# Kernel tuning notes

Measured on AMD Instinct MI355X. Metric: run time of the kernel, lower is better.

Reference implementation:

```python
import jax, jax.numpy as jnp
import numpy as np
from math import sqrt as msqrt

D_MODEL, D_FF, N_HEADS, D_K, D_V = 1024, 4096, 16, 64, 64
NEG = -1e9

def gelu_erf(x):
    return 0.5 * x * (1.0 + jax.lax.erf(x / msqrt(2.0)))

def layer_norm(x, g, b, eps=1e-5):
    mu = jnp.mean(x, axis=-1, keepdims=True)
    var = jnp.mean(jnp.square(x - mu), axis=-1, keepdims=True)
    return (x - mu) * jax.lax.rsqrt(var + eps) * g + b

def setup_inputs() -> dict:
    key = jax.random.key(0)
    ks = jax.random.split(key, 12)
    B, S = 2, 2048
    s = lambda fan_in: 1.0 / msqrt(fan_in)
    inp = {
        "x": jax.random.normal(ks[0], (B, S, D_MODEL), dtype=jnp.float32),
        "pad_mask": jnp.zeros((B, S, S), dtype=bool),
        "W_Q": jax.random.uniform(ks[1], (D_MODEL, N_HEADS * D_K), minval=-s(D_MODEL), maxval=s(D_MODEL)),
        "W_K": jax.random.uniform(ks[2], (D_MODEL, N_HEADS * D_K), minval=-s(D_MODEL), maxval=s(D_MODEL)),
        "W_V": jax.random.uniform(ks[3], (D_MODEL, N_HEADS * D_V), minval=-s(D_MODEL), maxval=s(D_MODEL)),
        "W_O": jax.random.uniform(ks[4], (N_HEADS * D_V, D_MODEL), minval=-s(N_HEADS * D_V), maxval=s(N_HEADS * D_V)),
        "fc1_w": jax.random.uniform(ks[5], (D_MODEL, D_FF), minval=-s(D_MODEL), maxval=s(D_MODEL)),
        "fc1_b": jax.random.uniform(ks[6], (D_FF,), minval=-s(D_MODEL), maxval=s(D_MODEL)),
        "fc2_w": jax.random.uniform(ks[7], (D_FF, D_MODEL), minval=-s(D_FF), maxval=s(D_FF)),
        "fc2_b": jax.random.uniform(ks[8], (D_MODEL,), minval=-s(D_FF), maxval=s(D_FF)),
        "ln1_g": jnp.ones((D_MODEL,), jnp.float32),
        "ln1_b": jnp.zeros((D_MODEL,), jnp.float32),
        "ln2_g": jnp.ones((D_MODEL,), jnp.float32),
        "ln2_b": jnp.zeros((D_MODEL,), jnp.float32),
    }
    return inp

def reference(x, pad_mask, W_Q, W_K, W_V, W_O, fc1_w, fc1_b, fc2_w, fc2_b,
              ln1_g, ln1_b, ln2_g, ln2_b):
    B, S, _ = x.shape
    # --- pre-norm MHA ---
    residual = x
    h = layer_norm(x, ln1_g, ln1_b)
    q = (h @ W_Q).reshape(B, S, N_HEADS, D_K).transpose(0, 2, 1, 3)  # [B,H,S,dk]
    k = (h @ W_K).reshape(B, S, N_HEADS, D_K).transpose(0, 2, 1, 3)
    v = (h @ W_V).reshape(B, S, N_HEADS, D_V).transpose(0, 2, 1, 3)
    scores = jnp.einsum("bhqd,bhkd->bhqk", q, k) / msqrt(D_K)
    scores = jnp.where(pad_mask[:, None, :, :], NEG, scores)
    attn = jax.nn.softmax(scores, axis=-1)
    ctx = jnp.einsum("bhqk,bhkd->bhqd", attn, v)
    ctx = ctx.transpose(0, 2, 1, 3).reshape(B, S, N_HEADS * D_V)
    x = ctx @ W_O + residual
    # --- pre-norm FFN (dropout is identity at inference) ---
    residual = x
    h = layer_norm(x, ln2_g, ln2_b)
    h = gelu_erf(h @ fc1_w + fc1_b)
    x = h @ fc2_w + fc2_b + residual
    return x
```

## Files before the change

kernel.cpp:

```cpp
#include <hip/hip_runtime.h>
#include <hip/hip_bf16.h>
#include <math.h>

#define DI __device__ __forceinline__

typedef short s16x8 __attribute__((ext_vector_type(8)));
typedef unsigned short u16x8_t __attribute__((ext_vector_type(8)));
typedef float f32x4 __attribute__((ext_vector_type(4)));

static constexpr int T_TOK = 4096;
static constexpr int DM    = 1024;
static constexpr int DFF   = 4096;
static constexpr int S_LEN = 2048;
static constexpr int NB    = 2;
static constexpr int LDQ   = 3072;

DI unsigned short f2bf(float f) {
    unsigned int u = __builtin_bit_cast(unsigned int, f);
    u += 0x7fffu + ((u >> 16) & 1u);
    return (unsigned short)(u >> 16);
}

DI float gelu_f(float x) {
    return 0.5f * x * (1.0f + erff(x * 0.70710678118654752440f));
}

DI int swz(int r) { return (r & 7) ^ ((r >> 3) & 7); }

DI void gload_lds16(const void* g, void* l) {
    __builtin_amdgcn_global_load_lds((const unsigned int*)g, (unsigned int*)l, 16, 0, 0);
}

__global__ __launch_bounds__(256) void tcvt_kernel(const float* __restrict__ in,
                                                   unsigned short* __restrict__ out,
                                                   int K, int N) {
    __shared__ float tile[32][33];
    const int tx = threadIdx.x & 31, ty = threadIdx.x >> 5;
    const int k0 = blockIdx.y * 32, n0 = blockIdx.x * 32;
#pragma unroll
    for (int i = 0; i < 4; ++i) {
        int k = ty + i * 8;
        tile[k][tx] = in[(size_t)(k0 + k) * N + n0 + tx];
    }
    __syncthreads();
#pragma unroll
    for (int i = 0; i < 4; ++i) {
        int n = ty + i * 8;
        out[(size_t)(n0 + n) * K + k0 + tx] = f2bf(tile[tx][n]);
    }
}

__global__ __launch_bounds__(256) void ln_kernel(const float* __restrict__ x,
                                                 const float* __restrict__ g,
                                                 const float* __restrict__ b,
                                                 unsigned short* __restrict__ out) {
    int row = blockIdx.x;
    int t = threadIdx.x;
    const float4 v = reinterpret_cast<const float4*>(x + (size_t)row * DM)[t];
    float s = v.x + v.y + v.z + v.w;
    float s2 = v.x * v.x + v.y * v.y + v.z * v.z + v.w * v.w;
#pragma unroll
    for (int m = 1; m < 64; m <<= 1) { s += __shfl_xor(s, m, 64); s2 += __shfl_xor(s2, m, 64); }
    __shared__ float red[8];
    int w = t >> 6;
    if ((t & 63) == 0) { red[w] = s; red[4 + w] = s2; }
    __syncthreads();
    s = red[0] + red[1] + red[2] + red[3];
    s2 = red[4] + red[5] + red[6] + red[7];
    float mu = s * (1.0f / DM);
    float var = s2 * (1.0f / DM) - mu * mu;
    float rs = rsqrtf(var + 1e-5f);
    float4 gv = reinterpret_cast<const float4*>(g)[t];
    float4 bv = reinterpret_cast<const float4*>(b)[t];
    ushort4 ov = make_ushort4(f2bf((v.x - mu) * rs * gv.x + bv.x),
                              f2bf((v.y - mu) * rs * gv.y + bv.y),
                              f2bf((v.z - mu) * rs * gv.z + bv.z),
                              f2bf((v.w - mu) * rs * gv.w + bv.w));
    reinterpret_cast<ushort4*>(out + (size_t)row * DM)[t] = ov;
}

template <int EPI>
__global__ __launch_bounds__(256) void gemm_kernel(const unsigned short* __restrict__ A,
                                                   const unsigned short* __restrict__ Bt,
                                                   const float* __restrict__ bias,
                                                   const float* __restrict__ resid,
                                                   void* __restrict__ Cv, int M, int N, int K) {
    __shared__ unsigned short Asm[128][32];
    __shared__ unsigned short Bsm[128][32];
    const int t = threadIdx.x, lane = t & 63, w = t >> 6;
    const int wr = w >> 1, wc = w & 1;
    const int m0 = blockIdx.y * 128, n0 = blockIdx.x * 128;
    const int c = lane & 15, g = lane >> 4;
    const int srow = lane >> 2, scol = (lane & 3) * 8;

    f32x4 acc[4][4] = {};
    const unsigned short* Ab = A + (size_t)m0 * K;
    const unsigned short* Bb = Bt + (size_t)n0 * K;

    for (int k0 = 0; k0 < K; k0 += 32) {
        __syncthreads();
#pragma unroll
        for (int cc = 0; cc < 2; ++cc) {
            int ch = 2 * w + cc;
            int r = ch * 16 + srow;
            gload_lds16(Ab + (size_t)r * K + k0 + scol, &Asm[ch * 16][0]);
            gload_lds16(Bb + (size_t)r * K + k0 + scol, &Bsm[ch * 16][0]);
        }
        __syncthreads();
        s16x8 af[4], bf[4];
#pragma unroll
        for (int i = 0; i < 4; ++i)
            af[i] = *reinterpret_cast<const s16x8*>(&Asm[wr * 64 + i * 16 + c][g * 8]);
#pragma unroll
        for (int n = 0; n < 4; ++n)
            bf[n] = *reinterpret_cast<const s16x8*>(&Bsm[wc * 64 + n * 16 + c][g * 8]);
#pragma unroll
        for (int i = 0; i < 4; ++i)
#pragma unroll
            for (int n = 0; n < 4; ++n)
                acc[i][n] = __builtin_amdgcn_mfma_f32_16x16x32_bf16(af[i], bf[n], acc[i][n], 0, 0, 0);
    }

    const int crow = g * 4;
#pragma unroll
    for (int i = 0; i < 4; ++i) {
#pragma unroll
        for (int n = 0; n < 4; ++n) {
            const int col = n0 + wc * 64 + n * 16 + c;
#pragma unroll
            for (int j = 0; j < 4; ++j) {
                const int row = m0 + wr * 64 + i * 16 + crow + j;
                float v = acc[i][n][j];
                if constexpr (EPI == 2) v = gelu_f(v + bias[col]);
                if constexpr (EPI == 3) v = v + bias[col] + resid[(size_t)row * N + col];
                if constexpr (EPI == 1) v = v + resid[(size_t)row * N + col];
                if constexpr (EPI == 4) v = (col < 1024) ? v * 0.125f : v;
                if constexpr (EPI == 2 || EPI == 4)
                    ((unsigned short*)Cv)[(size_t)row * N + col] = f2bf(v);
                else
                    ((float*)Cv)[(size_t)row * N + col] = v;
            }
        }
    }
}

__global__ __launch_bounds__(256) void attn_kernel(const unsigned short* __restrict__ QKV,
                                                   const unsigned char* __restrict__ mask,
                                                   unsigned short* __restrict__ O) {
    const int qt = blockIdx.x, h = blockIdx.y, b = blockIdx.z;
    const int t = threadIdx.x, lane = t & 63, w = t >> 6;
    const int c = lane & 15, g = lane >> 4;
    const int crow = g * 4;
    const int qb0 = qt * 64;
    const int qw = qb0 + w * 16;

    __shared__ unsigned short Ksm[64][64];
    __shared__ unsigned short VsmT[64][64];
    __shared__ unsigned short Psm[4][16][64];
    __shared__ unsigned char Msm[64][64];
    __shared__ int mflag[4];

    s16x8 qf[2];
    {
        const unsigned short* qp = QKV + (size_t)(b * S_LEN + qw + c) * LDQ + h * 64 + g * 8;
        qf[0] = *reinterpret_cast<const s16x8*>(qp);
        qf[1] = *reinterpret_cast<const s16x8*>(qp + 32);
    }

    float mrow[4] = {-3e38f, -3e38f, -3e38f, -3e38f};
    float lrow[4] = {0.f, 0.f, 0.f, 0.f};
    f32x4 oacc[4] = {};

    const int vtok = t >> 2;
    const int vd0 = (t & 3) * 16;
    const unsigned char* mbase = mask + (size_t)b * S_LEN * S_LEN + (size_t)(qb0 + vtok) * S_LEN + vd0;
    const unsigned short* kg = QKV + 1024;
    const unsigned short* vg = QKV + 2048;

    for (int kt = 0; kt < S_LEN; kt += 64) {
        __syncthreads();
#pragma unroll
        for (int cc = 0; cc < 2; ++cc) {
            int ch = 2 * w + cc;
            int r = ch * 8 + (lane >> 3);
            int slot = (lane & 7) ^ swz(r);
            gload_lds16(kg + (size_t)(b * S_LEN + kt + r) * LDQ + h * 64 + slot * 8,
                        &Ksm[ch * 8][0]);
        }
        u16x8_t v0, v1;
        {
            const unsigned short* vp = vg + (size_t)(b * S_LEN + kt + vtok) * LDQ + h * 64 + vd0;
            v0 = *reinterpret_cast<const u16x8_t*>(vp);
            v1 = *reinterpret_cast<const u16x8_t*>(vp + 8);
        }
        uint4 mv = *reinterpret_cast<const uint4*>(mbase + kt);
        unsigned mor = mv.x | mv.y | mv.z | mv.w;
        int anyw = __any(mor != 0);
        if (lane == 0) mflag[w] = anyw;
#pragma unroll
        for (int e = 0; e < 16; ++e) {
            int d = vd0 + e;
            unsigned short val = (e < 8) ? (unsigned short)v0[e] : (unsigned short)v1[e - 8];
            int byte = d * 128 + ((vtok * 2) ^ (swz(d) << 4));
            *(unsigned short*)((char*)&VsmT[0][0] + byte) = val;
        }
        __syncthreads();
        const int anym = mflag[0] | mflag[1] | mflag[2] | mflag[3];
        if (anym) {
            *reinterpret_cast<uint4*>(&Msm[vtok][vd0]) = mv;
            __syncthreads();
        }

        f32x4 s[4] = {};
#pragma unroll
        for (int kh = 0; kh < 2; ++kh) {
#pragma unroll
            for (int kb = 0; kb < 4; ++kb) {
                int key = kb * 16 + c;
                int byte = key * 128 + (((kh * 4 + g) ^ swz(key)) << 4);
                s16x8 kf = *(const s16x8*)((const char*)&Ksm[0][0] + byte);
                s[kb] = __builtin_amdgcn_mfma_f32_16x16x32_bf16(qf[kh], kf, s[kb], 0, 0, 0);
            }
        }
        if (anym) {
#pragma unroll
            for (int kb = 0; kb < 4; ++kb)
#pragma unroll
                for (int jr = 0; jr < 4; ++jr)
                    if (Msm[w * 16 + crow + jr][kb * 16 + c]) s[kb][jr] = -1e9f;
        }

        float corr[4];
#pragma unroll
        for (int jr = 0; jr < 4; ++jr) {
            float tm = fmaxf(fmaxf(s[0][jr], s[1][jr]), fmaxf(s[2][jr], s[3][jr]));
#pragma unroll
            for (int m = 1; m < 16; m <<= 1) tm = fmaxf(tm, __shfl_xor(tm, m, 16));
            float mnew = fmaxf(mrow[jr], tm);
            corr[jr] = __expf(mrow[jr] - mnew);
            mrow[jr] = mnew;
            float ps = 0.f;
#pragma unroll
            for (int kb = 0; kb < 4; ++kb) {
                float p = __expf(s[kb][jr] - mnew);
                s[kb][jr] = p;
                ps += p;
            }
#pragma unroll
            for (int m = 1; m < 16; m <<= 1) ps += __shfl_xor(ps, m, 16);
            lrow[jr] = lrow[jr] * corr[jr] + ps;
        }
#pragma unroll
        for (int nb = 0; nb < 4; ++nb)
#pragma unroll
            for (int jr = 0; jr < 4; ++jr) oacc[nb][jr] *= corr[jr];

#pragma unroll
        for (int kb = 0; kb < 4; ++kb)
#pragma unroll
            for (int jr = 0; jr < 4; ++jr) {
                int row = crow + jr;
                int byte = row * 128 + ((((kb * 16 + c) * 2)) ^ (swz(row) << 4));
                *(unsigned short*)((char*)&Psm[w][0][0] + byte) = f2bf(s[kb][jr]);
            }
#pragma unroll
        for (int kh = 0; kh < 2; ++kh) {
            int pbyte = c * 128 + (((kh * 4 + g) ^ swz(c)) << 4);
            s16x8 pf = *(const s16x8*)((const char*)&Psm[w][0][0] + pbyte);
#pragma unroll
            for (int nb = 0; nb < 4; ++nb) {
                int d = nb * 16 + c;
                int byte = d * 128 + (((kh * 4 + g) ^ swz(d)) << 4);
                s16x8 vf = *(const s16x8*)((const char*)&VsmT[0][0] + byte);
                oacc[nb] = __builtin_amdgcn_mfma_f32_16x16x32_bf16(pf, vf, oacc[nb], 0, 0, 0);
            }
        }
    }

    float inv[4];
#pragma unroll
    for (int jr = 0; jr < 4; ++jr) inv[jr] = lrow[jr] > 0.f ? 1.0f / lrow[jr] : 0.f;
#pragma unroll
    for (int nb = 0; nb < 4; ++nb) {
#pragma unroll
        for (int jr = 0; jr < 4; ++jr) {
            const size_t oo = (size_t)(b * S_LEN + qw + crow + jr) * DM + h * 64 + nb * 16 + c;
            O[oo] = f2bf(oacc[nb][jr] * inv[jr]);
        }
    }
}

extern "C" void kernel_launch(void* const* d_in, const int* in_sizes, int n_in,
                              void* d_out, int out_size, void* d_ws, size_t ws_size,
                              hipStream_t stream) {
    (void)in_sizes; (void)n_in; (void)out_size; (void)ws_size;
    const float* x   = (const float*)d_in[0];
    const unsigned char* mask = (const unsigned char*)d_in[1];
    const float* WQ  = (const float*)d_in[2];
    const float* WK  = (const float*)d_in[3];
    const float* WV  = (const float*)d_in[4];
    const float* WO  = (const float*)d_in[5];
    const float* F1W = (const float*)d_in[6];
    const float* F1B = (const float*)d_in[7];
    const float* F2W = (const float*)d_in[8];
    const float* F2B = (const float*)d_in[9];
    const float* L1G = (const float*)d_in[10];
    const float* L1B = (const float*)d_in[11];
    const float* L2G = (const float*)d_in[12];
    const float* L2B = (const float*)d_in[13];
    float* out = (float*)d_out;

    char* ws = (char*)d_ws;
    size_t off = 0;
    auto alloc = [&](size_t bytes) -> void* {
        void* p = ws + off;
        off += (bytes + 255) & ~(size_t)255;
        return p;
    };
    unsigned short* h1    = (unsigned short*)alloc((size_t)T_TOK * DM * 2);
    unsigned short* qkv   = (unsigned short*)alloc((size_t)T_TOK * LDQ * 2);
    unsigned short* ctx   = (unsigned short*)alloc((size_t)T_TOK * DM * 2);
    float*          x2    = (float*)alloc((size_t)T_TOK * DM * 4);
    unsigned short* h2    = (unsigned short*)alloc((size_t)T_TOK * DM * 2);
    unsigned short* h3    = (unsigned short*)alloc((size_t)T_TOK * DFF * 2);
    unsigned short* WQKVt = (unsigned short*)alloc((size_t)LDQ * DM * 2);
    unsigned short* WOt   = (unsigned short*)alloc((size_t)DM * DM * 2);
    unsigned short* F1Wt  = (unsigned short*)alloc((size_t)DFF * DM * 2);
    unsigned short* F2Wt  = (unsigned short*)alloc((size_t)DM * DFF * 2);

    dim3 t32(DM / 32, DM / 32);
    tcvt_kernel<<<t32, 256, 0, stream>>>(WQ, WQKVt, DM, DM);
    tcvt_kernel<<<t32, 256, 0, stream>>>(WK, WQKVt + (size_t)DM * DM, DM, DM);
    tcvt_kernel<<<t32, 256, 0, stream>>>(WV, WQKVt + (size_t)2 * DM * DM, DM, DM);
    tcvt_kernel<<<t32, 256, 0, stream>>>(WO, WOt, DM, DM);
    tcvt_kernel<<<dim3(DFF / 32, DM / 32), 256, 0, stream>>>(F1W, F1Wt, DM, DFF);
    tcvt_kernel<<<dim3(DM / 32, DFF / 32), 256, 0, stream>>>(F2W, F2Wt, DFF, DM);

    ln_kernel<<<T_TOK, 256, 0, stream>>>(x, L1G, L1B, h1);

    gemm_kernel<4><<<dim3(LDQ / 128, T_TOK / 128), 256, 0, stream>>>(h1, WQKVt, nullptr, nullptr,
                                                                     qkv, T_TOK, LDQ, DM);

    attn_kernel<<<dim3(S_LEN / 64, 16, NB), 256, 0, stream>>>(qkv, mask, ctx);

    gemm_kernel<1><<<dim3(DM / 128, T_TOK / 128), 256, 0, stream>>>(ctx, WOt, nullptr, x, x2,
                                                                    T_TOK, DM, DM);

    ln_kernel<<<T_TOK, 256, 0, stream>>>(x2, L2G, L2B, h2);

    gemm_kernel<2><<<dim3(DFF / 128, T_TOK / 128), 256, 0, stream>>>(h2, F1Wt, F1B, nullptr, h3,
                                                                     T_TOK, DFF, DM);
    gemm_kernel<3><<<dim3(DM / 128, T_TOK / 128), 256, 0, stream>>>(h3, F2Wt, F2B, x2, out,
                                                                    T_TOK, DM, DFF);
}
```

Before: 523.3 us.

## Write V transposed from QKV GEMM, double-buffer attention loads, narrow N-tiles for small GEMMs

The QKV GEMM epilogue now writes Q/K into a 2048-wide buffer and V transposed into a separate [dim][token] buffer. The attention kernel can then load V with async global-to-LDS copies instead of doing a per-element register transpose. Attention K/V tiles and mask loads are double-buffered so the next tile is fetched while the current one is computed. The N=1024 GEMMs (output projection and FC2) use 64-wide N tiles to launch twice as many blocks. Costs are strided scalar stores for the transposed V write and extra LDS for the double buffers.

New measurement: 522.9 us. About the same (-0.1%).

```diff
diff --git a/kernel.cpp b/kernel.cpp
--- a/kernel.cpp
+++ b/kernel.cpp
@@ -13,7 +13,7 @@
 static constexpr int DFF   = 4096;
 static constexpr int S_LEN = 2048;
 static constexpr int NB    = 2;
-static constexpr int LDQ   = 3072;
+static constexpr int LDK   = 2048;
 
 DI unsigned short f2bf(float f) {
     unsigned int u = __builtin_bit_cast(unsigned int, f);
@@ -79,21 +79,24 @@
     reinterpret_cast<ushort4*>(out + (size_t)row * DM)[t] = ov;
 }
 
-template <int EPI>
+template <int EPI, int BN>
 __global__ __launch_bounds__(256) void gemm_kernel(const unsigned short* __restrict__ A,
                                                    const unsigned short* __restrict__ Bt,
                                                    const float* __restrict__ bias,
                                                    const float* __restrict__ resid,
-                                                   void* __restrict__ Cv, int M, int N, int K) {
+                                                   void* __restrict__ Cv, void* __restrict__ Cv2,
+                                                   int M, int N, int K) {
+    constexpr int NN = BN / 32;
+    constexpr int BCH = BN / 64;
     __shared__ unsigned short Asm[128][32];
-    __shared__ unsigned short Bsm[128][32];
+    __shared__ unsigned short Bsm[BN][32];
     const int t = threadIdx.x, lane = t & 63, w = t >> 6;
     const int wr = w >> 1, wc = w & 1;
-    const int m0 = blockIdx.y * 128, n0 = blockIdx.x * 128;
+    const int m0 = blockIdx.y * 128, n0 = blockIdx.x * BN;
     const int c = lane & 15, g = lane >> 4;
     const int srow = lane >> 2, scol = (lane & 3) * 8;
 
-    f32x4 acc[4][4] = {};
+    f32x4 acc[4][NN] = {};
     const unsigned short* Ab = A + (size_t)m0 * K;
     const unsigned short* Bb = Bt + (size_t)n0 * K;
 
@@ -104,20 +107,25 @@
             int ch = 2 * w + cc;
             int r = ch * 16 + srow;
             gload_lds16(Ab + (size_t)r * K + k0 + scol, &Asm[ch * 16][0]);
+        }
+#pragma unroll
+        for (int cc = 0; cc < BCH; ++cc) {
+            int ch = BCH * w + cc;
+            int r = ch * 16 + srow;
             gload_lds16(Bb + (size_t)r * K + k0 + scol, &Bsm[ch * 16][0]);
         }
         __syncthreads();
-        s16x8 af[4], bf[4];
+        s16x8 af[4], bf[NN];
 #pragma unroll
         for (int i = 0; i < 4; ++i)
             af[i] = *reinterpret_cast<const s16x8*>(&Asm[wr * 64 + i * 16 + c][g * 8]);
 #pragma unroll
-        for (int n = 0; n < 4; ++n)
-            bf[n] = *reinterpret_cast<const s16x8*>(&Bsm[wc * 64 + n * 16 + c][g * 8]);
+        for (int n = 0; n < NN; ++n)
+            bf[n] = *reinterpret_cast<const s16x8*>(&Bsm[wc * (BN / 2) + n * 16 + c][g * 8]);
 #pragma unroll
         for (int i = 0; i < 4; ++i)
 #pragma unroll
-            for (int n = 0; n < 4; ++n)
+            for (int n = 0; n < NN; ++n)
                 acc[i][n] = __builtin_amdgcn_mfma_f32_16x16x32_bf16(af[i], bf[n], acc[i][n], 0, 0, 0);
     }
 
@@ -125,26 +133,36 @@
 #pragma unroll
     for (int i = 0; i < 4; ++i) {
 #pragma unroll
-        for (int n = 0; n < 4; ++n) {
-            const int col = n0 + wc * 64 + n * 16 + c;
+        for (int n = 0; n < NN; ++n) {
+            const int col = n0 + wc * (BN / 2) + n * 16 + c;
 #pragma unroll
             for (int j = 0; j < 4; ++j) {
                 const int row = m0 + wr * 64 + i * 16 + crow + j;
                 float v = acc[i][n][j];
-                if constexpr (EPI == 2) v = gelu_f(v + bias[col]);
-                if constexpr (EPI == 3) v = v + bias[col] + resid[(size_t)row * N + col];
-                if constexpr (EPI == 1) v = v + resid[(size_t)row * N + col];
-                if constexpr (EPI == 4) v = (col < 1024) ? v * 0.125f : v;
-                if constexpr (EPI == 2 || EPI == 4)
+                if constexpr (EPI == 2) {
+                    v = gelu_f(v + bias[col]);
                     ((unsigned short*)Cv)[(size_t)row * N + col] = f2bf(v);
-                else
+                } else if constexpr (EPI == 3) {
+                    v = v + bias[col] + resid[(size_t)row * N + col];
                     ((float*)Cv)[(size_t)row * N + col] = v;
-            }
-        }
-    }
-}
-
-__global__ __launch_bounds__(256) void attn_kernel(const unsigned short* __restrict__ QKV,
+                } else if constexpr (EPI == 1) {
+                    v = v + resid[(size_t)row * N + col];
+                    ((float*)Cv)[(size_t)row * N + col] = v;
+                } else {
+                    if (col < 2048) {
+                        float vv = (col < 1024) ? v * 0.125f : v;
+                        ((unsigned short*)Cv)[(size_t)row * LDK + col] = f2bf(vv);
+                    } else {
+                        ((unsigned short*)Cv2)[(size_t)(col - 2048) * T_TOK + row] = f2bf(v);
+                    }
+                }
+            }
+        }
+    }
+}
+
+__global__ __launch_bounds__(256) void attn_kernel(const unsigned short* __restrict__ QK,
+                                                   const unsigned short* __restrict__ Vt,
                                                    const unsigned char* __restrict__ mask,
                                                    unsigned short* __restrict__ O) {
     const int qt = blockIdx.x, h = blockIdx.y, b = blockIdx.z;
@@ -154,15 +172,14 @@
     const int qb0 = qt * 64;
     const int qw = qb0 + w * 16;
 
-    __shared__ unsigned short Ksm[64][64];
-    __shared__ unsigned short VsmT[64][64];
+    __shared__ unsigned short Ksm[2][64][64];
+    __shared__ unsigned short Vsm[2][64][64];
     __shared__ unsigned short Psm[4][16][64];
     __shared__ unsigned char Msm[64][64];
-    __shared__ int mflag[4];
 
     s16x8 qf[2];
     {
-        const unsigned short* qp = QKV + (size_t)(b * S_LEN + qw + c) * LDQ + h * 64 + g * 8;
+        const unsigned short* qp = QK + (size_t)(b * S_LEN + qw + c) * LDK + h * 64 + g * 8;
         qf[0] = *reinterpret_cast<const s16x8*>(qp);
         qf[1] = *reinterpret_cast<const s16x8*>(qp + 32);
     }
@@ -173,42 +190,39 @@
 
     const int vtok = t >> 2;
     const int vd0 = (t & 3) * 16;
-    const unsigned char* mbase = mask + (size_t)b * S_LEN * S_LEN + (size_t)(qb0 + vtok) * S_LEN + vd0;
-    const unsigned short* kg = QKV + 1024;
-    const unsigned short* vg = QKV + 2048;
-
-    for (int kt = 0; kt < S_LEN; kt += 64) {
-        __syncthreads();
+    const unsigned char* mcol = mask + (size_t)b * S_LEN * S_LEN + (size_t)(qb0 + vtok) * S_LEN + vd0;
+    const unsigned short* kg = QK + 1024;
+    const int srow8 = lane >> 3, sslot = lane & 7;
+
+    auto stage = [&](int buf, int kt) {
 #pragma unroll
         for (int cc = 0; cc < 2; ++cc) {
             int ch = 2 * w + cc;
-            int r = ch * 8 + (lane >> 3);
-            int slot = (lane & 7) ^ swz(r);
-            gload_lds16(kg + (size_t)(b * S_LEN + kt + r) * LDQ + h * 64 + slot * 8,
-                        &Ksm[ch * 8][0]);
-        }
-        u16x8_t v0, v1;
-        {
-            const unsigned short* vp = vg + (size_t)(b * S_LEN + kt + vtok) * LDQ + h * 64 + vd0;
-            v0 = *reinterpret_cast<const u16x8_t*>(vp);
-            v1 = *reinterpret_cast<const u16x8_t*>(vp + 8);
-        }
-        uint4 mv = *reinterpret_cast<const uint4*>(mbase + kt);
-        unsigned mor = mv.x | mv.y | mv.z | mv.w;
-        int anyw = __any(mor != 0);
-        if (lane == 0) mflag[w] = anyw;
-#pragma unroll
-        for (int e = 0; e < 16; ++e) {
-            int d = vd0 + e;
-            unsigned short val = (e < 8) ? (unsigned short)v0[e] : (unsigned short)v1[e - 8];
-            int byte = d * 128 + ((vtok * 2) ^ (swz(d) << 4));
-            *(unsigned short*)((char*)&VsmT[0][0] + byte) = val;
-        }
+            int r = ch * 8 + srow8;
+            int slot = sslot ^ swz(r);
+            gload_lds16(kg + (size_t)(b * S_LEN + kt + r) * LDK + h * 64 + slot * 8,
+                        &Ksm[buf][ch * 8][0]);
+            gload_lds16(Vt + (size_t)(h * 64 + r) * T_TOK + b * S_LEN + kt + slot * 8,
+                        &Vsm[buf][ch * 8][0]);
+        }
+    };
+
+    stage(0, 0);
+    uint4 mv0 = *reinterpret_cast<const uint4*>(mcol);
+    asm volatile("s_waitcnt vmcnt(0)" ::: "memory");
+    int anym = __syncthreads_or((mv0.x | mv0.y | mv0.z | mv0.w) != 0);
+    if (anym) {
+        *reinterpret_cast<uint4*>(&Msm[vtok][vd0]) = mv0;
         __syncthreads();
-        const int anym = mflag[0] | mflag[1] | mflag[2] | mflag[3];
-        if (anym) {
-            *reinterpret_cast<uint4*>(&Msm[vtok][vd0]) = mv;
-            __syncthreads();
+    }
+
+    constexpr int NT = S_LEN / 64;
+    for (int it = 0; it < NT; ++it) {
+        const int cur = it & 1;
+        uint4 mv = {0u, 0u, 0u, 0u};
+        if (it < NT - 1) {
+            stage(cur ^ 1, (it + 1) * 64);
+            mv = *reinterpret_cast<const uint4*>(mcol + (it + 1) * 64);
         }
 
         f32x4 s[4] = {};
@@ -218,7 +232,7 @@
             for (int kb = 0; kb < 4; ++kb) {
                 int key = kb * 16 + c;
                 int byte = key * 128 + (((kh * 4 + g) ^ swz(key)) << 4);
-                s16x8 kf = *(const s16x8*)((const char*)&Ksm[0][0] + byte);
+                s16x8 kf = *(const s16x8*)((const char*)&Ksm[cur][0][0] + byte);
                 s[kb] = __builtin_amdgcn_mfma_f32_16x16x32_bf16(qf[kh], kf, s[kb], 0, 0, 0);
             }
         }
@@ -260,7 +274,7 @@
 #pragma unroll
             for (int jr = 0; jr < 4; ++jr) {
                 int row = crow + jr;
-                int byte = row * 128 + ((((kb * 16 + c) * 2)) ^ (swz(row) << 4));
+                int byte = row * 128 + (((kb * 16 + c) * 2) ^ (swz(row) << 4));
                 *(unsigned short*)((char*)&Psm[w][0][0] + byte) = f2bf(s[kb][jr]);
             }
 #pragma unroll
@@ -271,10 +285,18 @@
             for (int nb = 0; nb < 4; ++nb) {
                 int d = nb * 16 + c;
                 int byte = d * 128 + (((kh * 4 + g) ^ swz(d)) << 4);
-                s16x8 vf = *(const s16x8*)((const char*)&VsmT[0][0] + byte);
+                s16x8 vf = *(const s16x8*)((const char*)&Vsm[cur][0][0] + byte);
                 oacc[nb] = __builtin_amdgcn_mfma_f32_16x16x32_bf16(pf, vf, oacc[nb], 0, 0, 0);
             }
         }
+
+        asm volatile("s_waitcnt vmcnt(0)" ::: "memory");
+        int nxt = __syncthreads_or((mv.x | mv.y | mv.z | mv.w) != 0);
+        if (nxt) {
+            *reinterpret_cast<uint4*>(&Msm[vtok][vd0]) = mv;
+            __syncthreads();
+        }
+        anym = nxt;
     }
 
     float inv[4];
@@ -318,12 +340,13 @@
         return p;
     };
     unsigned short* h1    = (unsigned short*)alloc((size_t)T_TOK * DM * 2);
-    unsigned short* qkv   = (unsigned short*)alloc((size_t)T_TOK * LDQ * 2);
+    unsigned short* qk    = (unsigned short*)alloc((size_t)T_TOK * LDK * 2);
+    unsigned short* vt    = (unsigned short*)alloc((size_t)DM * T_TOK * 2);
     unsigned short* ctx   = (unsigned short*)alloc((size_t)T_TOK * DM * 2);
     float*          x2    = (float*)alloc((size_t)T_TOK * DM * 4);
     unsigned short* h2    = (unsigned short*)alloc((size_t)T_TOK * DM * 2);
     unsigned short* h3    = (unsigned short*)alloc((size_t)T_TOK * DFF * 2);
-    unsigned short* WQKVt = (unsigned short*)alloc((size_t)LDQ * DM * 2);
+    unsigned short* WQKVt = (unsigned short*)alloc((size_t)3 * DM * DM * 2);
     unsigned short* WOt   = (unsigned short*)alloc((size_t)DM * DM * 2);
     unsigned short* F1Wt  = (unsigned short*)alloc((size_t)DFF * DM * 2);
     unsigned short* F2Wt  = (unsigned short*)alloc((size_t)DM * DFF * 2);
@@ -338,18 +361,18 @@
 
     ln_kernel<<<T_TOK, 256, 0, stream>>>(x, L1G, L1B, h1);
 
-    gemm_kernel<4><<<dim3(LDQ / 128, T_TOK / 128), 256, 0, stream>>>(h1, WQKVt, nullptr, nullptr,
-                                                                     qkv, T_TOK, LDQ, DM);
-
-    attn_kernel<<<dim3(S_LEN / 64, 16, NB), 256, 0, stream>>>(qkv, mask, ctx);
-
-    gemm_kernel<1><<<dim3(DM / 128, T_TOK / 128), 256, 0, stream>>>(ctx, WOt, nullptr, x, x2,
-                                                                    T_TOK, DM, DM);
+    gemm_kernel<4, 128><<<dim3(3072 / 128, T_TOK / 128), 256, 0, stream>>>(
+        h1, WQKVt, nullptr, nullptr, qk, vt, T_TOK, 3072, DM);
+
+    attn_kernel<<<dim3(S_LEN / 64, 16, NB), 256, 0, stream>>>(qk, vt, mask, ctx);
+
+    gemm_kernel<1, 64><<<dim3(DM / 64, T_TOK / 128), 256, 0, stream>>>(
+        ctx, WOt, nullptr, x, x2, nullptr, T_TOK, DM, DM);
 
     ln_kernel<<<T_TOK, 256, 0, stream>>>(x2, L2G, L2B, h2);
 
-    gemm_kernel<2><<<dim3(DFF / 128, T_TOK / 128), 256, 0, stream>>>(h2, F1Wt, F1B, nullptr, h3,
-                                                                     T_TOK, DFF, DM);
-    gemm_kernel<3><<<dim3(DM / 128, T_TOK / 128), 256, 0, stream>>>(h3, F2Wt, F2B, x2, out,
-                                                                    T_TOK, DM, DFF);
-}
+    gemm_kernel<2, 128><<<dim3(DFF / 128, T_TOK / 128), 256, 0, stream>>>(
+        h2, F1Wt, F1B, nullptr, h3, nullptr, T_TOK, DFF, DM);
+    gemm_kernel<3, 64><<<dim3(DM / 64, T_TOK / 128), 256, 0, stream>>>(
+        h3, F2Wt, F2B, x2, out, nullptr, T_TOK, DM, DFF);
+}
```
